# Optimization experiments

Measured on AMD Instinct MI355X. Metric: run time of the kernel, lower is better.

The kernel has to match this reference:

```python
import jax, jax.numpy as jnp
import numpy as np

VOCAB, EMBED, HIDDEN, OUT = 1024, 512, 1024, 1024
B, T = 1024, 32


def setup_inputs() -> dict:
    key = jax.random.key(0)
    ks = jax.random.split(key, 10)
    s_emb = 1.0 / np.sqrt(VOCAB)
    s_ih = 1.0 / np.sqrt(HIDDEN)  # PyTorch RNNCell init scale uses hidden_size
    s_out = 1.0 / np.sqrt(HIDDEN)
    return {
        "message": jax.random.normal(ks[0], (B, T, VOCAB), dtype=jnp.float32),
        "W_emb": jax.random.uniform(ks[1], (EMBED, VOCAB), jnp.float32, -s_emb, s_emb),
        "b_emb": jax.random.uniform(ks[2], (EMBED,), jnp.float32, -s_emb, s_emb),
        "W_ih": jax.random.uniform(ks[3], (HIDDEN, EMBED), jnp.float32, -s_ih, s_ih),
        "b_ih": jax.random.uniform(ks[4], (HIDDEN,), jnp.float32, -s_ih, s_ih),
        "W_hh": jax.random.uniform(ks[5], (HIDDEN, HIDDEN), jnp.float32, -s_ih, s_ih),
        "b_hh": jax.random.uniform(ks[6], (HIDDEN,), jnp.float32, -s_ih, s_ih),
        "W_out": jax.random.uniform(ks[7], (OUT, HIDDEN), jnp.float32, -s_out, s_out),
        "b_out": jax.random.uniform(ks[8], (OUT,), jnp.float32, -s_out, s_out),
    }


def reference(message, W_emb, b_emb, W_ih, b_ih, W_hh, b_hh, W_out, b_out):
    # emb: [B, T, E] -- Linear embedding of (relaxed one-hot) message
    emb = jnp.einsum("btv,ev->bte", message, W_emb) + b_emb
    # Precompute input projections for all steps at once: [T, B, H]
    x_proj = jnp.einsum("bte,he->tbh", emb, W_ih) + b_ih

    def step(h, x_t):
        h_new = jnp.tanh(x_t + h @ W_hh.T + b_hh)
        return h_new, None

    h0 = jnp.zeros((message.shape[0], W_hh.shape[0]), dtype=message.dtype)
    h_T, _ = jax.lax.scan(step, h0, x_proj)
    out = h_T @ W_out.T + b_out  # [B, OUT]
    return out  # agent is identity here
```

## Files before the change

### kernel.cpp

```cpp
#include <hip/hip_runtime.h>
#include <cstdint>
#include <cstddef>

#define B_DIM 1024
#define T_DIM 32
#define V_DIM 1024
#define E_DIM 512
#define H_DIM 1024
#define O_DIM 1024

typedef unsigned short u16;
typedef __attribute__((ext_vector_type(8))) __bf16 bf16x8;
typedef __attribute__((ext_vector_type(4))) float f32x4;

__device__ __forceinline__ float bf2f(u16 u) {
  union { unsigned int i; float f; } v; v.i = ((unsigned int)u) << 16; return v.f;
}
__device__ __forceinline__ u16 f2bf(float f) {
  union { float f; unsigned int i; } v; v.f = f;
  return (u16)((v.i + 0x7fffu + ((v.i >> 16) & 1u)) >> 16);
}
__device__ __forceinline__ void async_cp16(const void* g, void* l) {
  __builtin_amdgcn_global_load_lds(
      (const __attribute__((address_space(1))) void*)g,
      (__attribute__((address_space(3))) void*)l, 16, 0, 0);
}
__device__ __forceinline__ float fast_tanh(float v) {
  return 1.f - 2.f / (__expf(2.f * v) + 1.f);
}

__global__ __launch_bounds__(256) void prep_all(
    const float* __restrict__ Whh, const float* __restrict__ Wout,
    const float* __restrict__ msg, const float* __restrict__ Wih,
    const float* __restrict__ Wemb, const float* __restrict__ bemb,
    const float* __restrict__ bih, u16* __restrict__ dWhh,
    u16* __restrict__ dWout, u16* __restrict__ dmsg,
    u16* __restrict__ Wc, float* __restrict__ bc) {
  __shared__ __align__(16) float As[16][68];
  __shared__ __align__(16) float Bs[16][68];
  const int bid = blockIdx.x;
  if (bid < 2048) {
    const int QW = 262144;
    const int QM = 8388608;
    const int total = dmsg ? (2 * QW + QM) : (2 * QW);
    int i = bid * 256 + threadIdx.x;
    const int stride = 2048 * 256;
    for (; i < total; i += stride) {
      const float4* src; ushort4* dst; int j;
      if (i < QW)          { src = (const float4*)Whh;  dst = (ushort4*)dWhh;  j = i; }
      else if (i < 2 * QW) { src = (const float4*)Wout; dst = (ushort4*)dWout; j = i - QW; }
      else                 { src = (const float4*)msg;  dst = (ushort4*)dmsg;  j = i - 2 * QW; }
      float4 v = src[j];
      ushort4 o = {f2bf(v.x), f2bf(v.y), f2bf(v.z), f2bf(v.w)};
      dst[j] = o;
    }
  } else if (bid < 2304) {
    const int b2 = bid - 2048;
    const int tx = threadIdx.x & 15, ty = threadIdx.x >> 4;
    const int v0 = (b2 & 15) * 64, h0 = (b2 >> 4) * 64;
    float acc[4][4] = {};
    for (int kt = 0; kt < 32; ++kt) {
#pragma unroll
      for (int i = 0; i < 4; ++i) {
        int idx = threadIdx.x + i * 256;
        int row = idx >> 4, k = idx & 15;
        As[k][row] = Wih[(size_t)(h0 + row) * E_DIM + kt * 16 + k];
        Bs[k][row] = Wemb[(size_t)(kt * 16 + k) * V_DIM + v0 + row];
      }
      __syncthreads();
      for (int k = 0; k < 16; ++k) {
        float4 a = *(const float4*)&As[k][ty * 4];
        float4 b = *(const float4*)&Bs[k][tx * 4];
        const float av[4] = {a.x, a.y, a.z, a.w}, bv[4] = {b.x, b.y, b.z, b.w};
#pragma unroll
        for (int i = 0; i < 4; ++i)
#pragma unroll
          for (int j = 0; j < 4; ++j) acc[i][j] += av[i] * bv[j];
      }
      __syncthreads();
    }
#pragma unroll
    for (int i = 0; i < 4; ++i)
#pragma unroll
      for (int j = 0; j < 4; ++j)
        Wc[(size_t)(h0 + ty * 4 + i) * V_DIM + v0 + tx * 4 + j] = f2bf(acc[i][j]);
  } else {
    int h = (bid - 2304) * 256 + threadIdx.x;
    float s = 0.f;
    for (int e = 0; e < E_DIM; ++e) s += Wih[(size_t)h * E_DIM + e] * bemb[e];
    bc[h] = s + bih[h];
  }
}

__global__ __launch_bounds__(256) void gemm_xp(
    const u16* __restrict__ A, const u16* __restrict__ Bm,
    const float* __restrict__ bias, const float* __restrict__ bhh,
    u16* __restrict__ outp) {
  __shared__ __align__(16) u16 lds[32768];
  const int tid = threadIdx.x, lane = tid & 63, w = tid >> 6;
  const int lrow = lane >> 4, lcol = lane & 15;
  const int l7 = lane & 7, r8 = lane >> 3;
  const int p = blockIdx.x;
  const int xk = p & 7, q = p >> 3;
  const int mt = xk * 32 + (q >> 3), nt = q & 7;
  const int m0 = mt * 128, n0 = nt * 128;
  const int mq = (w & 1) * 64, nq = (w >> 1) * 64;
  const int half = w >> 1, wv = w & 1;

  auto stage = [&](int kk, int d) {
    const u16* src = half ? Bm : A;
    const int rbase = half ? n0 : m0;
#pragma unroll
    for (int i = 0; i < 8; ++i) {
      int row = wv * 64 + i * 8 + r8;
      async_cp16(src + (size_t)(rbase + row) * H_DIM + kk * 64 + ((l7 ^ r8) << 3),
                 lds + d * 16384 + half * 8192 + (wv * 64 + i * 8) * 64);
    }
  };

  f32x4 acc[4][4] = {};
  auto kchunk = [&](int d) {
    const u16* base = lds + d * 16384;
#pragma unroll
    for (int ks = 0; ks < 2; ++ks) {
      const int ce = ks * 32 + lrow * 8;
      bf16x8 a[4], b[4];
#pragma unroll
      for (int i = 0; i < 4; ++i) {
        int row = mq + i * 16 + lcol;
        a[i] = *(const bf16x8*)(base + row * 64 + (ce ^ ((row & 7) << 3)));
      }
#pragma unroll
      for (int i = 0; i < 4; ++i) {
        int row = nq + i * 16 + lcol;
        b[i] = *(const bf16x8*)(base + 8192 + row * 64 + (ce ^ ((row & 7) << 3)));
      }
#pragma unroll
      for (int i = 0; i < 4; ++i)
#pragma unroll
        for (int j = 0; j < 4; ++j)
          acc[i][j] = __builtin_amdgcn_mfma_f32_16x16x32_bf16(a[i], b[j], acc[i][j], 0, 0, 0);
    }
  };

  stage(0, 0); stage(1, 1);
#pragma unroll
  for (int kk = 0; kk < 16; ++kk) {
    if (kk <= 14) asm volatile("s_waitcnt vmcnt(8)" ::: "memory");
    else          asm volatile("s_waitcnt vmcnt(0)" ::: "memory");
    __builtin_amdgcn_s_barrier();
    kchunk(kk & 1);
    __builtin_amdgcn_s_barrier();
    if (kk <= 13) stage(kk + 2, kk & 1);
  }

  float bv[4], bh[4];
#pragma unroll
  for (int j = 0; j < 4; ++j) {
    bv[j] = bias[n0 + nq + j * 16 + lcol];
    bh[j] = bhh[n0 + nq + j * 16 + lcol];
  }
#pragma unroll
  for (int i = 0; i < 4; ++i)
#pragma unroll
    for (int rr = 0; rr < 4; ++rr) {
      int rg = m0 + mq + i * 16 + lrow * 4 + rr;
      int bI = rg >> 5, tI = rg & 31;
      u16* dst = outp + ((size_t)tI * B_DIM + bI) * H_DIM + n0 + nq;
      if (tI == 0) {
#pragma unroll
        for (int j = 0; j < 4; ++j)
          dst[j * 16 + lcol] = f2bf(fast_tanh(acc[i][j][rr] + bv[j] + bh[j]));
      } else {
#pragma unroll
        for (int j = 0; j < 4; ++j)
          dst[j * 16 + lcol] = f2bf(acc[i][j][rr] + bv[j]);
      }
    }
}

template <int MODE>
__global__ __launch_bounds__(256) void step64(
    const u16* __restrict__ A, const u16* __restrict__ Bm,
    const u16* __restrict__ x, const float* __restrict__ bias,
    void* __restrict__ outp) {
  constexpr int XOFF = 24576;
  constexpr int LDSE = (MODE == 1) ? 28672 : 24576;
  __shared__ __align__(16) u16 lds[LDSE];
  const int tid = threadIdx.x, lane = tid & 63, w = tid >> 6;
  const int lrow = lane >> 4, lcol = lane & 15;
  const int l7 = lane & 7, r8 = lane >> 3;
  const int p = blockIdx.x;
  const int xcd = p & 7, q = p >> 3;
  const int mt = xcd * 2 + (q >> 4), nt = q & 15;
  const int m0 = mt * 64, n0 = nt * 64;
  const int mq = (w & 1) * 32, nq = (w >> 1) * 32;
  const int half = w >> 1, wv = w & 1;

  auto stage = [&](int kk, int d) {
    const u16* src = half ? Bm : A;
    const int rbase = half ? n0 : m0;
#pragma unroll
    for (int i = 0; i < 4; ++i) {
      int row = wv * 32 + i * 8 + r8;
      async_cp16(src + (size_t)(rbase + row) * H_DIM + kk * 64 + ((l7 ^ r8) << 3),
                 lds + d * 8192 + half * 4096 + (wv * 32 + i * 8) * 64);
    }
  };
  auto stage_x = [&]() {
#pragma unroll
    for (int i = 0; i < 2; ++i)
      async_cp16(x + (size_t)(m0 + i * 32 + w * 8 + r8) * H_DIM + n0 + l7 * 8,
                 lds + XOFF + (i * 32 + w * 8) * 64);
  };

  f32x4 acc[2][2] = {};
  auto kchunk = [&](int d) {
    const u16* base = lds + d * 8192;
#pragma unroll
    for (int ks = 0; ks < 2; ++ks) {
      const int ce = ks * 32 + lrow * 8;
      bf16x8 a[2], b[2];
#pragma unroll
      for (int i = 0; i < 2; ++i) {
        int row = mq + i * 16 + lcol;
        a[i] = *(const bf16x8*)(base + row * 64 + (ce ^ ((row & 7) << 3)));
      }
#pragma unroll
      for (int j = 0; j < 2; ++j) {
        int row = nq + j * 16 + lcol;
        b[j] = *(const bf16x8*)(base + 4096 + row * 64 + (ce ^ ((row & 7) << 3)));
      }
#pragma unroll
      for (int i = 0; i < 2; ++i)
#pragma unroll
        for (int j = 0; j < 2; ++j)
          acc[i][j] = __builtin_amdgcn_mfma_f32_16x16x32_bf16(a[i], b[j], acc[i][j], 0, 0, 0);
    }
  };

  if (A != nullptr) {
    if (MODE == 1) stage_x();
    stage(0, 0); stage(1, 1); stage(2, 2);
#pragma unroll
    for (int kk = 0; kk < 16; ++kk) {
      if (kk <= 13)      asm volatile("s_waitcnt vmcnt(8)" ::: "memory");
      else if (kk == 14) asm volatile("s_waitcnt vmcnt(4)" ::: "memory");
      else               asm volatile("s_waitcnt vmcnt(0)" ::: "memory");
      __builtin_amdgcn_s_barrier();
      kchunk(kk % 3);
      __builtin_amdgcn_s_barrier();
      if (kk <= 12) stage(kk + 3, kk % 3);
    }
  } else {
    if (MODE == 1) stage_x();
    asm volatile("s_waitcnt vmcnt(0)" ::: "memory");
    __builtin_amdgcn_s_barrier();
  }

  float bv[2] = {bias[n0 + nq + lcol], bias[n0 + nq + 16 + lcol]};
  if (MODE == 2) {
#pragma unroll
    for (int i = 0; i < 2; ++i)
#pragma unroll
      for (int rr = 0; rr < 4; ++rr) {
        int row = m0 + mq + i * 16 + lrow * 4 + rr;
#pragma unroll
        for (int j = 0; j < 2; ++j)
          ((float*)outp)[(size_t)row * O_DIM + n0 + nq + j * 16 + lcol] =
              acc[i][j][rr] + bv[j];
      }
  } else {
#pragma unroll
    for (int i = 0; i < 2; ++i)
#pragma unroll
      for (int rr = 0; rr < 4; ++rr) {
        int rowl = mq + i * 16 + lrow * 4 + rr;
#pragma unroll
        for (int j = 0; j < 2; ++j) {
          int col = nq + j * 16 + lcol;
          float v = acc[i][j][rr] + bv[j] + bf2f(lds[XOFF + rowl * 64 + col]);
          lds[rowl * 64 + col] = f2bf(fast_tanh(v));
        }
      }
    __syncthreads();
    {
      int row = tid >> 2, c = (tid & 3) * 16;
      const uint4* s = (const uint4*)(lds + row * 64 + c);
      uint4 v0 = s[0], v1 = s[1];
      uint4* g = (uint4*)((u16*)outp + (size_t)(m0 + row) * H_DIM + n0 + c);
      g[0] = v0;
      g[1] = v1;
    }
  }
}

__global__ __launch_bounds__(256) void xproj_mfma(
    const float* __restrict__ msg, const u16* __restrict__ Wc,
    const float* __restrict__ bc, u16* __restrict__ xp) {
  __shared__ u16 As[128 * 64];
  __shared__ u16 Bs[128 * 64];
  const int tid = threadIdx.x, lane = tid & 63, w = tid >> 6;
  const int lrow = lane >> 4, lcol = lane & 15;
  const int p = blockIdx.y * gridDim.x + blockIdx.x;
  const int xk = p & 7, q = p >> 3;
  const int m0 = (xk * 32 + (q >> 3)) * 128;
  const int n0 = (q & 7) * 128;
  const int mq = (w & 1) * 64, nq = (w >> 1) * 64;
  f32x4 acc[4][4] = {};
  const int r8 = lane >> 3, l7 = lane & 7;
  const int ar = tid >> 1, ak = (tid & 1) * 32;

  auto stageB = [&](int kk) {
#pragma unroll
    for (int i = 0; i < 4; ++i) {
      int ch = w * 4 + i;
      async_cp16(Wc + (size_t)(n0 + ch * 8 + r8) * V_DIM + kk * 64 + ((l7 ^ r8) << 3),
                 Bs + ch * 512);
    }
  };
  float4 areg[8];
  auto loadA = [&](int kk) {
    const float4* src = (const float4*)(msg + (size_t)(m0 + ar) * V_DIM + kk * 64 + ak);
#pragma unroll
    for (int i = 0; i < 8; ++i) areg[i] = src[i];
  };
  auto writeA = [&]() {
    u16 tmp[32];
#pragma unroll
    for (int i = 0; i < 8; ++i) {
      tmp[i * 4 + 0] = f2bf(areg[i].x);
      tmp[i * 4 + 1] = f2bf(areg[i].y);
      tmp[i * 4 + 2] = f2bf(areg[i].z);
      tmp[i * 4 + 3] = f2bf(areg[i].w);
    }
#pragma unroll
    for (int i = 0; i < 4; ++i) {
      int c = (ak + i * 8) ^ ((ar & 7) << 3);
      *(uint4*)(As + (size_t)ar * 64 + c) = *(const uint4*)(tmp + i * 8);
    }
  };

  loadA(0);
  stageB(0);
  writeA();
  for (int kk = 0; kk < 16; ++kk) {
    __syncthreads();
    if (kk < 15) loadA(kk + 1);
#pragma unroll
    for (int ks = 0; ks < 2; ++ks) {
      const int kb = ks * 32 + lrow * 8;
      bf16x8 a[4], b[4];
#pragma unroll
      for (int i = 0; i < 4; ++i) {
        int row = mq + i * 16 + lcol;
        a[i] = *(const bf16x8*)(As + row * 64 + (kb ^ ((row & 7) << 3)));
      }
#pragma unroll
      for (int i = 0; i < 4; ++i) {
        int row = nq + i * 16 + lcol;
        b[i] = *(const bf16x8*)(Bs + row * 64 + (kb ^ ((row & 7) << 3)));
      }
#pragma unroll
      for (int i = 0; i < 4; ++i)
#pragma unroll
        for (int j = 0; j < 4; ++j)
          acc[i][j] = __builtin_amdgcn_mfma_f32_16x16x32_bf16(a[i], b[j], acc[i][j], 0, 0, 0);
    }
    __syncthreads();
    if (kk < 15) { stageB(kk + 1); writeA(); }
  }
  float bcv[4];
#pragma unroll
  for (int j = 0; j < 4; ++j) bcv[j] = bc[n0 + nq + j * 16 + lcol];
#pragma unroll
  for (int i = 0; i < 4; ++i)
#pragma unroll
    for (int rr = 0; rr < 4; ++rr) {
      int rg = m0 + mq + i * 16 + lrow * 4 + rr;
      int bI = rg >> 5, tI = rg & 31;
      u16* dst = xp + ((size_t)tI * B_DIM + bI) * H_DIM + n0 + nq;
#pragma unroll
      for (int j = 0; j < 4; ++j)
        dst[j * 16 + lcol] = f2bf(acc[i][j][rr] + bcv[j]);
    }
}

extern "C" void kernel_launch(void* const* d_in, const int* in_sizes, int n_in,
                              void* d_out, int out_size, void* d_ws, size_t ws_size,
                              hipStream_t stream) {
  const float* msg  = (const float*)d_in[0];
  const float* Wemb = (const float*)d_in[1];
  const float* bemb = (const float*)d_in[2];
  const float* Wih  = (const float*)d_in[3];
  const float* bih  = (const float*)d_in[4];
  const float* Whh  = (const float*)d_in[5];
  const float* bhh  = (const float*)d_in[6];
  const float* Wout = (const float*)d_in[7];
  const float* bout = (const float*)d_in[8];
  char* ws = (char*)d_ws;

  float* bc   = (float*)ws;
  u16* Wc     = (u16*)(ws + 4096);
  u16* Whh_b  = (u16*)(ws + 2101248);
  u16* Wout_b = (u16*)(ws + 4198400);
  u16* hA     = (u16*)(ws + 6295552);
  u16* hB     = (u16*)(ws + 8392704);
  u16* xp     = (u16*)(ws + 10489856);
  u16* msgb   = (u16*)(ws + 77598720);
  const size_t NEED_SMALL = 77598720;
  const size_t NEED_BIG   = 77598720 + 67108864;
  if (ws_size < NEED_SMALL) return;
  const bool big = ws_size >= NEED_BIG;

  prep_all<<<2308, 256, 0, stream>>>(Whh, Wout, big ? msg : nullptr, Wih, Wemb,
                                     bemb, bih, Whh_b, Wout_b,
                                     big ? msgb : nullptr, Wc, bc);

  if (big) {
    gemm_xp<<<2048, 256, 0, stream>>>(msgb, Wc, bc, bhh, xp);
    step64<1><<<256, 256, 0, stream>>>(xp, Whh_b,
                                       xp + (size_t)1 * B_DIM * H_DIM, bhh, hB);
    for (int t = 2; t < 32; ++t) {
      const u16* hin = (t & 1) ? hA : hB;
      u16* hout = (t & 1) ? hB : hA;
      step64<1><<<256, 256, 0, stream>>>(hin, Whh_b,
                                         xp + (size_t)t * B_DIM * H_DIM, bhh, hout);
    }
  } else {
    xproj_mfma<<<dim3(8, 256), 256, 0, stream>>>(msg, Wc, bc, xp);
    step64<1><<<256, 256, 0, stream>>>(nullptr, Whh_b, xp, bhh, hA);
    for (int t = 1; t < 32; ++t) {
      const u16* hin = (t & 1) ? hA : hB;
      u16* hout = (t & 1) ? hB : hA;
      step64<1><<<256, 256, 0, stream>>>(hin, Whh_b,
                                         xp + (size_t)t * B_DIM * H_DIM, bhh, hout);
    }
  }
  step64<2><<<256, 256, 0, stream>>>(hB, Wout_b, nullptr, bout, d_out);
}
```

Baseline: 546.8 us.

## Compute combined Wih·Wemb weight with split-bf16 MFMA GEMM instead of FP32 SIMT

Replaces the FP32 scalar tiled GEMM that builds the combined weight Wc = W_ih·W_emb inside prep_all with a separate MFMA kernel. Operands are split into bf16 hi/lo parts and concatenated along K (hi·hi + lo·hi + hi·lo), so the GEMM keeps near-FP32 accuracy while using bf16 matrix cores. prep_all now only writes the split operands, transposing W_emb through shared memory. The cost is an extra kernel launch and a 3x longer K, and the temporaries reuse the xp workspace region before xp is written.

```diff
diff --git a/kernel.cpp b/kernel.cpp
--- a/kernel.cpp
+++ b/kernel.cpp
@@ -35,15 +35,14 @@
     const float* __restrict__ Wemb, const float* __restrict__ bemb,
     const float* __restrict__ bih, u16* __restrict__ dWhh,
     u16* __restrict__ dWout, u16* __restrict__ dmsg,
-    u16* __restrict__ Wc, float* __restrict__ bc) {
-  __shared__ __align__(16) float As[16][68];
-  __shared__ __align__(16) float Bs[16][68];
-  const int bid = blockIdx.x;
+    u16* __restrict__ A3, u16* __restrict__ B3, float* __restrict__ bc) {
+  __shared__ __align__(16) float T[64][65];
+  const int bid = blockIdx.x, tid = threadIdx.x;
   if (bid < 2048) {
     const int QW = 262144;
     const int QM = 8388608;
     const int total = dmsg ? (2 * QW + QM) : (2 * QW);
-    int i = bid * 256 + threadIdx.x;
+    int i = bid * 256 + tid;
     const int stride = 2048 * 256;
     for (; i < total; i += stride) {
       const float4* src; ushort4* dst; int j;
@@ -54,42 +53,112 @@
       ushort4 o = {f2bf(v.x), f2bf(v.y), f2bf(v.z), f2bf(v.w)};
       dst[j] = o;
     }
+  } else if (bid < 2176) {
+    const int b8 = bid - 2048;
+    const float4* W4 = (const float4*)Wih;
+#pragma unroll
+    for (int it = 0; it < 4; ++it) {
+      int i = it * 256 + tid;
+      int r = b8 * 8 + (i >> 7), c4 = i & 127;
+      float4 v = W4[(size_t)r * 128 + c4];
+      ushort4 hi = {f2bf(v.x), f2bf(v.y), f2bf(v.z), f2bf(v.w)};
+      ushort4 lo = {f2bf(v.x - bf2f(hi.x)), f2bf(v.y - bf2f(hi.y)),
+                    f2bf(v.z - bf2f(hi.z)), f2bf(v.w - bf2f(hi.w))};
+      u16* base = A3 + (size_t)r * 1536 + c4 * 4;
+      *(ushort4*)(base)        = hi;
+      *(ushort4*)(base + 512)  = lo;
+      *(ushort4*)(base + 1024) = hi;
+    }
   } else if (bid < 2304) {
-    const int b2 = bid - 2048;
-    const int tx = threadIdx.x & 15, ty = threadIdx.x >> 4;
-    const int v0 = (b2 & 15) * 64, h0 = (b2 >> 4) * 64;
-    float acc[4][4] = {};
-    for (int kt = 0; kt < 32; ++kt) {
-#pragma unroll
-      for (int i = 0; i < 4; ++i) {
-        int idx = threadIdx.x + i * 256;
-        int row = idx >> 4, k = idx & 15;
-        As[k][row] = Wih[(size_t)(h0 + row) * E_DIM + kt * 16 + k];
-        Bs[k][row] = Wemb[(size_t)(kt * 16 + k) * V_DIM + v0 + row];
-      }
-      __syncthreads();
-      for (int k = 0; k < 16; ++k) {
-        float4 a = *(const float4*)&As[k][ty * 4];
-        float4 b = *(const float4*)&Bs[k][tx * 4];
-        const float av[4] = {a.x, a.y, a.z, a.w}, bv[4] = {b.x, b.y, b.z, b.w};
-#pragma unroll
-        for (int i = 0; i < 4; ++i)
-#pragma unroll
-          for (int j = 0; j < 4; ++j) acc[i][j] += av[i] * bv[j];
-      }
-      __syncthreads();
-    }
-#pragma unroll
-    for (int i = 0; i < 4; ++i)
-#pragma unroll
-      for (int j = 0; j < 4; ++j)
-        Wc[(size_t)(h0 + ty * 4 + i) * V_DIM + v0 + tx * 4 + j] = f2bf(acc[i][j]);
+    const int b = bid - 2176;
+    const int e0 = (b >> 4) * 64, v0 = (b & 15) * 64;
+#pragma unroll
+    for (int ps = 0; ps < 16; ++ps) {
+      int r = ps * 4 + (tid >> 6), c = tid & 63;
+      T[r][c] = Wemb[(size_t)(e0 + r) * V_DIM + v0 + c];
+    }
+    __syncthreads();
+#pragma unroll
+    for (int ps = 0; ps < 16; ++ps) {
+      int vr = ps * 4 + (tid >> 6), ec = tid & 63;
+      float wv = T[ec][vr];
+      u16 hi = f2bf(wv);
+      u16 lo = f2bf(wv - bf2f(hi));
+      u16* base = B3 + (size_t)(v0 + vr) * 1536 + e0 + ec;
+      base[0]    = hi;
+      base[512]  = hi;
+      base[1024] = lo;
+    }
   } else {
-    int h = (bid - 2304) * 256 + threadIdx.x;
+    int h = (bid - 2304) * 256 + tid;
     float s = 0.f;
     for (int e = 0; e < E_DIM; ++e) s += Wih[(size_t)h * E_DIM + e] * bemb[e];
     bc[h] = s + bih[h];
   }
+}
+
+__global__ __launch_bounds__(256) void wcomb_mfma(
+    const u16* __restrict__ A3, const u16* __restrict__ B3,
+    u16* __restrict__ Wc) {
+  __shared__ __align__(16) u16 lds[24576];
+  const int tid = threadIdx.x, lane = tid & 63, w = tid >> 6;
+  const int lrow = lane >> 4, lcol = lane & 15;
+  const int l7 = lane & 7, r8 = lane >> 3;
+  const int p = blockIdx.x;
+  const int xcd = p & 7, q = p >> 3;
+  const int mt = xcd * 2 + (q >> 4), nt = q & 15;
+  const int m0 = mt * 64, n0 = nt * 64;
+  const int mq = (w & 1) * 32, nq = (w >> 1) * 32;
+  const int half = w >> 1, wv = w & 1;
+
+  auto stage = [&](int kk, int d) {
+    const u16* src = half ? B3 : A3;
+    const int rbase = half ? n0 : m0;
+#pragma unroll
+    for (int i = 0; i < 4; ++i) {
+      int row = wv * 32 + i * 8 + r8;
+      async_cp16(src + (size_t)(rbase + row) * 1536 + kk * 64 + ((l7 ^ r8) << 3),
+                 lds + d * 8192 + half * 4096 + (wv * 32 + i * 8) * 64);
+    }
+  };
+  f32x4 acc[2][2] = {};
+  auto kchunk = [&](int d) {
+    const u16* base = lds + d * 8192;
+#pragma unroll
+    for (int ks = 0; ks < 2; ++ks) {
+      const int ce = ks * 32 + lrow * 8;
+      int rA0 = mq + lcol, rA1 = mq + 16 + lcol;
+      int rB0 = nq + lcol, rB1 = nq + 16 + lcol;
+      bf16x8 a0 = *(const bf16x8*)(base + rA0 * 64 + (ce ^ ((rA0 & 7) << 3)));
+      bf16x8 a1 = *(const bf16x8*)(base + rA1 * 64 + (ce ^ ((rA1 & 7) << 3)));
+      bf16x8 b0 = *(const bf16x8*)(base + 4096 + rB0 * 64 + (ce ^ ((rB0 & 7) << 3)));
+      bf16x8 b1 = *(const bf16x8*)(base + 4096 + rB1 * 64 + (ce ^ ((rB1 & 7) << 3)));
+      acc[0][0] = __builtin_amdgcn_mfma_f32_16x16x32_bf16(a0, b0, acc[0][0], 0, 0, 0);
+      acc[0][1] = __builtin_amdgcn_mfma_f32_16x16x32_bf16(a0, b1, acc[0][1], 0, 0, 0);
+      acc[1][0] = __builtin_amdgcn_mfma_f32_16x16x32_bf16(a1, b0, acc[1][0], 0, 0, 0);
+      acc[1][1] = __builtin_amdgcn_mfma_f32_16x16x32_bf16(a1, b1, acc[1][1], 0, 0, 0);
+    }
+  };
+  stage(0, 0); stage(1, 1); stage(2, 2);
+#pragma unroll
+  for (int kk = 0; kk < 24; ++kk) {
+    if (kk <= 21)      asm volatile("s_waitcnt vmcnt(8)" ::: "memory");
+    else if (kk == 22) asm volatile("s_waitcnt vmcnt(4)" ::: "memory");
+    else               asm volatile("s_waitcnt vmcnt(0)" ::: "memory");
+    __builtin_amdgcn_s_barrier();
+    kchunk(kk % 3);
+    __builtin_amdgcn_s_barrier();
+    if (kk <= 20) stage(kk + 3, kk % 3);
+  }
+#pragma unroll
+  for (int i = 0; i < 2; ++i)
+#pragma unroll
+    for (int rr = 0; rr < 4; ++rr) {
+      int hrow = m0 + mq + i * 16 + lrow * 4 + rr;
+#pragma unroll
+      for (int j = 0; j < 2; ++j)
+        Wc[(size_t)hrow * V_DIM + n0 + nq + j * 16 + lcol] = f2bf(acc[i][j][rr]);
+    }
 }
 
 __global__ __launch_bounds__(256) void gemm_xp(
@@ -408,6 +477,8 @@
   u16* hB     = (u16*)(ws + 8392704);
   u16* xp     = (u16*)(ws + 10489856);
   u16* msgb   = (u16*)(ws + 77598720);
+  u16* A3     = (u16*)(ws + 10489856);
+  u16* B3     = (u16*)(ws + 10489856 + 3145728);
   const size_t NEED_SMALL = 77598720;
   const size_t NEED_BIG   = 77598720 + 67108864;
   if (ws_size < NEED_SMALL) return;
@@ -415,7 +486,8 @@
 
   prep_all<<<2308, 256, 0, stream>>>(Whh, Wout, big ? msg : nullptr, Wih, Wemb,
                                      bemb, bih, Whh_b, Wout_b,
-                                     big ? msgb : nullptr, Wc, bc);
+                                     big ? msgb : nullptr, A3, B3, bc);
+  wcomb_mfma<<<256, 256, 0, stream>>>(A3, B3, Wc);
 
   if (big) {
     gemm_xp<<<2048, 256, 0, stream>>>(msgb, Wc, bc, bhh, xp);
```

Result: faster. 509.1 us (-6.9%).
